# Kernel tuning notes

Measured on AMD Instinct MI355X. Metric: run time of the kernel, lower is better.

## Reference

```python
import jax, jax.numpy as jnp
import numpy as np

B, K, D, H = 4, 2048, 1024, 16
NCTX = K // 2
IMAGE_SIZE = 224
MAX_POS = 1024


def _build_rope_cache_2d(max_pos, dim, base=10000.0):
    half_dim = dim // 2
    theta = 1.0 / base ** (np.arange(0, half_dim, 2, dtype=np.float32) / half_dim)
    positions = np.arange(max_pos, dtype=np.float32)
    freqs = np.outer(positions, theta)  # [max_pos, dim/4]
    return jnp.asarray(np.stack([np.cos(freqs), np.sin(freqs)], axis=-1))  # [max_pos, dim/4, 2]


def apply_rope_2d(x, coords, rope_cache, image_size):
    b, k, d = x.shape
    half, quarter = d // 2, d // 4
    max_pos = rope_cache.shape[0]
    cn = jnp.clip(coords / image_size * (max_pos - 1), 0, max_pos - 1)
    y_pos = cn[..., 0].astype(jnp.int32)
    x_pos = cn[..., 1].astype(jnp.int32)
    y_rope = rope_cache[y_pos]  # [b,k,quarter,2]
    x_rope = rope_cache[x_pos]

    def rot(part, r):
        c, s = r[..., 0], r[..., 1]
        p0, p1 = part[..., 0], part[..., 1]
        return jnp.stack([p0 * c - p1 * s, p0 * s + p1 * c], -1).reshape(b, k, half)

    xp = x[..., :half].reshape(b, k, quarter, 2)
    yp = x[..., half:].reshape(b, k, quarter, 2)
    return jnp.concatenate([rot(xp, x_rope), rot(yp, y_rope)], -1)


def mha(q_tok, kv_tok, in_w, in_b, out_w, out_b, num_heads):
    b, nq, d = q_tok.shape
    hd = d // num_heads
    wq, wk, wv = jnp.split(in_w, 3, axis=0)
    bq, bk, bv = jnp.split(in_b, 3)
    q = (q_tok @ wq.T + bq).reshape(b, nq, num_heads, hd)
    k = (kv_tok @ wk.T + bk).reshape(b, -1, num_heads, hd)
    v = (kv_tok @ wv.T + bv).reshape(b, -1, num_heads, hd)
    s = jnp.einsum('bqhd,bkhd->bhqk', q, k) / jnp.sqrt(jnp.asarray(hd, q.dtype))
    a = jax.nn.softmax(s, axis=-1)
    o = jnp.einsum('bhqk,bkhd->bqhd', a, v).reshape(b, nq, d)
    return o @ out_w.T + out_b


def setup_inputs() -> dict:
    key = jax.random.key(0)
    ks = jax.random.split(key, 12)
    sc = 1.0 / np.sqrt(D)
    x = jax.random.normal(ks[0], (B, K, D), jnp.float32)
    coords = jax.random.uniform(ks[1], (B, K, 2), jnp.float32) * IMAGE_SIZE
    # boolean context mask with exactly NCTX context tokens per batch (code assumes equal counts)
    perms = jax.vmap(lambda k_: jax.random.permutation(k_, K))(jax.random.split(ks[2], B))
    is_context = jax.vmap(lambda m, i: m.at[i].set(True))(jnp.zeros((B, K), bool), perms[:, :NCTX])
    rope_cache = _build_rope_cache_2d(MAX_POS, D)
    return {
        'x': x, 'coords': coords, 'is_context': is_context, 'rope_cache': rope_cache,
        'ctx_in_w': jax.random.normal(ks[3], (3 * D, D), jnp.float32) * sc,
        'ctx_in_b': jnp.zeros((3 * D,), jnp.float32),
        'ctx_out_w': jax.random.normal(ks[4], (D, D), jnp.float32) * sc,
        'ctx_out_b': jnp.zeros((D,), jnp.float32),
        'tgt_in_w': jax.random.normal(ks[5], (3 * D, D), jnp.float32) * sc,
        'tgt_in_b': jnp.zeros((3 * D,), jnp.float32),
        'tgt_out_w': jax.random.normal(ks[6], (D, D), jnp.float32) * sc,
        'tgt_out_b': jnp.zeros((D,), jnp.float32),
    }


def reference(x, coords, is_context, rope_cache,
              ctx_in_w, ctx_in_b, ctx_out_w, ctx_out_b,
              tgt_in_w, tgt_in_b, tgt_out_w, tgt_out_b):
    # 2D RoPE before attention (as in the backbone)
    xr = apply_rope_2d(x, coords, rope_cache, IMAGE_SIZE)
    # stable argsort: context positions (key 0) first, in original order
    order = jnp.argsort(jnp.where(is_context, 0, 1), axis=1, stable=True)
    ctx_idx = order[:, :NCTX]   # [B, NCTX]
    tgt_idx = order[:, NCTX:]   # [B, K-NCTX]
    ctx_tok = jnp.take_along_axis(xr, ctx_idx[..., None], axis=1)
    tgt_tok = jnp.take_along_axis(xr, tgt_idx[..., None], axis=1)
    ctx_out = mha(ctx_tok, ctx_tok, ctx_in_w, ctx_in_b, ctx_out_w, ctx_out_b, H)
    tgt_out = mha(tgt_tok, ctx_tok, tgt_in_w, tgt_in_b, tgt_out_w, tgt_out_b, H)
    out = jnp.zeros_like(x)
    out = jax.vmap(lambda o, i, v: o.at[i].set(v))(out, ctx_idx, ctx_out)
    out = jax.vmap(lambda o, i, v: o.at[i].set(v))(out, tgt_idx, tgt_out)
    return out
```

## Files before the change

kernel.cpp:

```cpp
#include <hip/hip_runtime.h>
#include <math.h>

#define B_    4
#define K_    2048
#define D_    1024
#define H_    16
#define NCTX_ 1024

typedef unsigned short ushort_t;
typedef _Float16 f16;
typedef __attribute__((ext_vector_type(8))) _Float16 f16x8;
typedef __attribute__((ext_vector_type(4))) float f32x4;

union U4 {
  f16 h[4];
  ushort4 u;
};

union P4 {
  f16 h[4];
  ushort4 u;
};

__device__ __forceinline__ void gload16(const void* g, void* l) {
  __builtin_amdgcn_global_load_lds(
      (const __attribute__((address_space(1))) unsigned int*)g,
      (__attribute__((address_space(3))) unsigned int*)l, 16, 0, 0);
}

__global__ __launch_bounds__(256) void partition_kernel(
    const unsigned char* __restrict__ isctx, int* __restrict__ pos,
    int* __restrict__ ipos) {
  const int b = blockIdx.x;
  const int tid = threadIdx.x;
  const int wid = tid >> 6, lane = tid & 63;
  __shared__ int csum[4];
  __shared__ int waveTot[4];
  __shared__ int strideSh;

  int cnt = 0;
  for (int i = 0; i < 32; ++i) cnt += (isctx[tid * 32 + i] != 0);
  for (int off = 32; off; off >>= 1) cnt += __shfl_down(cnt, off, 64);
  if (lane == 0) csum[wid] = cnt;
  __syncthreads();
  if (tid == 0) {
    int t = csum[0] + csum[1] + csum[2] + csum[3];
    strideSh = (t > 2048) ? 1 : ((t > 768) ? 4 : 8);
  }
  __syncthreads();
  const int stride = strideSh;

  const unsigned char* base = isctx + (size_t)b * K_ * stride;
  int f[8];
  int s = 0;
  for (int i = 0; i < 8; ++i) {
    f[i] = base[(size_t)(tid * 8 + i) * stride] != 0;
    s += f[i];
  }
  int inc = s;
  for (int off = 1; off < 64; off <<= 1) {
    int v = __shfl_up(inc, off, 64);
    if (lane >= off) inc += v;
  }
  if (lane == 63) waveTot[wid] = inc;
  __syncthreads();
  int wOff = 0;
  for (int w = 0; w < wid; ++w) wOff += waveTot[w];
  int run = wOff + inc - s;
  for (int i = 0; i < 8; ++i) {
    int k = tid * 8 + i;
    int p;
    if (f[i]) {
      p = run;
      run++;
    } else {
      p = NCTX_ + k - run;
    }
    pos[b * K_ + k] = p;
    ipos[b * K_ + p] = k;
  }
}

__global__ __launch_bounds__(256) void rope_kernel(
    const float* __restrict__ x, const float* __restrict__ coords,
    const float* __restrict__ cache, const int* __restrict__ ipos,
    f16* __restrict__ tok) {
  const int row = blockIdx.x;
  const int b = row >> 11;
  const int r = row & (K_ - 1);
  const int k = ipos[row];
  const int t = threadIdx.x;

  const float cy = coords[(size_t)(b * K_ + k) * 2 + 0];
  const float cx = coords[(size_t)(b * K_ + k) * 2 + 1];
  const int ypos = (int)fminf(fmaxf(cy / 224.0f * 1023.0f, 0.0f), 1023.0f);
  const int xpos = (int)fminf(fmaxf(cx / 224.0f * 1023.0f, 0.0f), 1023.0f);

  const float4 v = ((const float4*)(x + ((size_t)b * K_ + k) * D_))[t];
  const int e = 4 * t;
  const float* crow;
  int coff;
  if (e < 512) {
    crow = cache + (size_t)xpos * 512;
    coff = e;
  } else {
    crow = cache + (size_t)ypos * 512;
    coff = e - 512;
  }
  const float4 cs = *(const float4*)(crow + coff);
  float o[4];
  o[0] = v.x * cs.x - v.y * cs.y;
  o[1] = v.x * cs.y + v.y * cs.x;
  o[2] = v.z * cs.z - v.w * cs.w;
  o[3] = v.z * cs.w + v.w * cs.z;
  U4 h;
#pragma unroll
  for (int i = 0; i < 4; ++i) h.h[i] = (f16)o[i];
  ((ushort4*)(tok + ((size_t)b * K_ + r) * D_))[t] = h.u;
}

__global__ __launch_bounds__(256) void cvt_all(
    const float* __restrict__ ctx_in_w, const float* __restrict__ tgt_in_w,
    const float* __restrict__ ctx_out_w, const float* __restrict__ tgt_out_w,
    f16* __restrict__ dst) {
  const int i4 = blockIdx.x * 256 + threadIdx.x;
  const int f = i4 * 4;
  const float* src;
  if (f < 3145728) src = ctx_in_w + f;
  else if (f < 5242880) src = tgt_in_w + (f - 3145728 + 1048576);
  else if (f < 6291456) src = tgt_in_w + (f - 5242880);
  else if (f < 7340032) src = ctx_out_w + (f - 6291456);
  else src = tgt_out_w + (f - 7340032);
  const float4 v = *(const float4*)src;
  U4 u;
  u.h[0] = (f16)v.x;
  u.h[1] = (f16)v.y;
  u.h[2] = (f16)v.z;
  u.h[3] = (f16)v.w;
  ((ushort4*)dst)[i4] = u.u;
}

#define GEMM_PRE(AP, WP, Kd)                                                  \
  const int rb_ = wave * 8 + (lane >> 3);          \
  const int kk_ = ((lane & 7) ^ (lane >> 3)) * 8;   \
  const f16* gA_ = (AP) + (size_t)rb_ * (Kd) + kk_;                           \
  const f16* gW_ = (WP) + (size_t)rb_ * (Kd) + kk_;                           \
  const int lA_ = wave * 8 * 64 + lane * 8;

#define GEMM_STAGE(k0s, bb)                                                   \
  _Pragma("unroll") for (int j = 0; j < 4; ++j) {                             \
    gload16(gA_ + (size_t)j * 32 * Kd_ + (k0s), &lds[(bb) + j * 2048 + lA_]); \
    gload16(gW_ + (size_t)j * 32 * Kd_ + (k0s),                               \
            &lds[(bb) + 8192 + j * 2048 + lA_]);                              \
  }

#define GEMM_TILE(bb)                                                         \
  _Pragma("unroll") for (int kh = 0; kh < 2; ++kh) {                          \
    f16x8 af[4], wf[4];                                                       \
    _Pragma("unroll") for (int i = 0; i < 4; ++i) {                           \
      const int ca = ((kh * 4 + quad) ^ (m16 & 7)) * 8;                       \
      af[i] = *(const f16x8*)&lds[(bb) + (wm + i * 16 + m16) * 64 + ca];      \
      wf[i] =                                                                 \
          *(const f16x8*)&lds[(bb) + 8192 + (wn + i * 16 + m16) * 64 + ca];   \
    }                                                                         \
    _Pragma("unroll") for (int i = 0; i < 4; ++i)                             \
        _Pragma("unroll") for (int j = 0; j < 4; ++j)                         \
      acc[i][j] = __builtin_amdgcn_mfma_f32_16x16x32_f16(af[i], wf[j],        \
                                                         acc[i][j], 0, 0, 0); \
  }

#define GEMM_CORE(AP, WP, Kd)                                                 \
  f32x4 acc[4][4];                                                            \
  {                                                                           \
    const f32x4 z = {0.f, 0.f, 0.f, 0.f};                                     \
    for (int i = 0; i < 4; ++i)                                               \
      for (int j = 0; j < 4; ++j) acc[i][j] = z;                              \
  }                                                                           \
  const int Kd_ = (Kd);                                                       \
  GEMM_PRE(AP, WP, Kd_)                                                       \
  GEMM_STAGE(0, 0)                                                            \
  for (int t = 0; t < Kd_ / 64; ++t) {                                        \
    const int cb = (t & 1) * 16384;                                           \
    if (t + 1 < Kd_ / 64) {                                                   \
      GEMM_STAGE((t + 1) * 64, ((t + 1) & 1) * 16384)                         \
      asm volatile("s_waitcnt vmcnt(8)" ::: "memory");                        \
    } else {                                                                  \
      asm volatile("s_waitcnt vmcnt(0)" ::: "memory");                        \
    }                                                                         \
    __builtin_amdgcn_s_barrier();                                             \
    asm volatile("" ::: "memory");                                            \
    GEMM_TILE(cb)                                                             \
    asm volatile("" ::: "memory");                                            \
    __builtin_amdgcn_s_barrier();                                             \
  }

__global__ __launch_bounds__(256, 2) void gemm_proj(
    const f16* __restrict__ tok, const f16* __restrict__ wcat,
    const float* __restrict__ ctx_in_b, const float* __restrict__ tgt_in_b,
    f16* __restrict__ qkvc, f16* __restrict__ kvt, f16* __restrict__ qt,
    f16* __restrict__ vtc, f16* __restrict__ vtt) {
  __shared__ f16 lds[32768];
  const int tid = threadIdx.x;
  const int wave = tid >> 6, lane = tid & 63;
  const int quad = lane >> 4, m16 = lane & 15;
  const int nb = blockIdx.x, mb = blockIdx.y, b = blockIdx.z;
  const int wm = (wave & 1) << 6, wn = (wave >> 1) << 6;
  const int m0 = mb * 128;
  const bool isQ = nb >= 40;
  const int n0 = isQ ? (nb - 40) * 128 : nb * 128;
  const f16* AP = tok + (size_t)b * K_ * D_ +
                  (isQ ? (size_t)NCTX_ * D_ : (size_t)0) + (size_t)m0 * D_;
  const f16* WP = wcat + (isQ ? (size_t)5242880 : (size_t)0) +
                  (size_t)n0 * D_;

  GEMM_CORE(AP, WP, D_)

#pragma unroll
  for (int j = 0; j < 4; ++j) {
    const int col = n0 + wn + j * 16 + m16;
    if (isQ) {
      const float bv = tgt_in_b[col];
      f16* dst = qt + (size_t)b * NCTX_ * 1024;
#pragma unroll
      for (int i = 0; i < 4; ++i) {
        const int mr = m0 + wm + i * 16 + quad * 4;
#pragma unroll
        for (int r = 0; r < 4; ++r)
          dst[(size_t)(mr + r) * 1024 + col] = (f16)(acc[i][j][r] + bv);
      }
    } else if (col < 2048) {
      const float bv = ctx_in_b[col];
      f16* dst = qkvc + (size_t)b * NCTX_ * 2048;
#pragma unroll
      for (int i = 0; i < 4; ++i) {
        const int mr = m0 + wm + i * 16 + quad * 4;
#pragma unroll
        for (int r = 0; r < 4; ++r)
          dst[(size_t)(mr + r) * 2048 + col] = (f16)(acc[i][j][r] + bv);
      }
    } else if (col >= 3072 && col < 4096) {
      const float bv = tgt_in_b[D_ + col - 3072];
      f16* dst = kvt + (size_t)b * NCTX_ * 1024;
      const int dcol = col - 3072;
#pragma unroll
      for (int i = 0; i < 4; ++i) {
        const int mr = m0 + wm + i * 16 + quad * 4;
#pragma unroll
        for (int r = 0; r < 4; ++r)
          dst[(size_t)(mr + r) * 1024 + dcol] = (f16)(acc[i][j][r] + bv);
      }
    } else {
      const bool isCtxV = col < 3072;
      const int hd = isCtxV ? (col - 2048) : (col - 4096);
      const float bv = isCtxV ? ctx_in_b[col] : tgt_in_b[D_ + col - 3072];
      f16* dst = (isCtxV ? vtc : vtt) +
                 ((size_t)(b * H_ + (hd >> 6)) << 16) +
                 (size_t)(hd & 63) * 1024;
#pragma unroll
      for (int i = 0; i < 4; ++i) {
        const int mr = m0 + wm + i * 16 + quad * 4;
        P4 p4;
#pragma unroll
        for (int r = 0; r < 4; ++r) p4.h[r] = (f16)(acc[i][j][r] + bv);
        *(ushort4*)(dst + mr) = p4.u;
      }
    }
  }
}

__global__ __launch_bounds__(256, 2) void gemm_out(
    const f16* __restrict__ Atok, const f16* __restrict__ Wbase,
    const float* __restrict__ bias_ctx, const float* __restrict__ bias_tgt,
    const int* __restrict__ ipos, float* __restrict__ out) {
  __shared__ f16 lds[32768];
  const int tid = threadIdx.x;
  const int wave = tid >> 6, lane = tid & 63;
  const int quad = lane >> 4, m16 = lane & 15;
  const int n0 = blockIdx.x * 128, m0 = blockIdx.y * 128;
  const int b = blockIdx.z & 3, sel = blockIdx.z >> 2;
  const int wm = (wave & 1) << 6, wn = (wave >> 1) << 6;
  const f16* AP = Atok + (size_t)b * K_ * D_ + (size_t)sel * NCTX_ * D_ +
                  (size_t)m0 * D_;
  const f16* WP = Wbase + (size_t)sel * 1048576 + (size_t)n0 * D_;
  const float* bias = sel ? bias_tgt : bias_ctx;

  GEMM_CORE(AP, WP, D_)

#pragma unroll
  for (int j = 0; j < 4; ++j) {
    const int col = n0 + wn + j * 16 + m16;
    const float bv = bias[col];
#pragma unroll
    for (int i = 0; i < 4; ++i) {
      const int mr = m0 + wm + i * 16 + quad * 4;
#pragma unroll
      for (int r = 0; r < 4; ++r) {
        const int orow = ipos[b * K_ + sel * NCTX_ + mr + r];
        out[(size_t)b * K_ * D_ + (size_t)orow * D_ + col] =
            acc[i][j][r] + bv;
      }
    }
  }
}

__global__ __launch_bounds__(512) void attn_mfma(
    const f16* __restrict__ qkvc, const f16* __restrict__ kvt,
    const f16* __restrict__ qt, const f16* __restrict__ vtc,
    const f16* __restrict__ vtt, f16* __restrict__ O) {
  __shared__ f16 QP[8192];
  __shared__ f16 Ks[2][4096];
  __shared__ f16 Vs[2][4096];
  const int tid = threadIdx.x, wave = tid >> 6, lane = tid & 63;
  const int quad = lane >> 4, m16 = lane & 15;
  const int q0 = blockIdx.x * 128, h = blockIdx.y;
  const int zz = blockIdx.z;
  const int b = zz & 3;
  const bool isCtx = zz < 4;

  const f16* Qb;
  const f16* Kb;
  int ld;
  if (isCtx) {
    Qb = qkvc + (size_t)b * NCTX_ * 2048 + h * 64;
    Kb = Qb + 1024;
    ld = 2048;
  } else {
    Qb = qt + (size_t)b * NCTX_ * 1024 + h * 64;
    Kb = kvt + (size_t)b * NCTX_ * 1024 + h * 64;
    ld = 1024;
  }
  const f16* Vb = (isCtx ? vtc : vtt) + ((size_t)(b * H_ + h) << 16);
  f16* Ob = O + (size_t)b * K_ * D_ + (isCtx ? 0 : (size_t)NCTX_ * D_);

  const int rowS = tid >> 3;
  const int kkc = ((tid & 7) ^ (rowS & 7)) * 8;
  const int lB = tid * 8;

#pragma unroll
  for (int j = 0; j < 2; ++j)
    gload16(Qb + (size_t)(q0 + j * 64 + rowS) * ld + kkc, &QP[j * 4096 + lB]);
  gload16(Kb + (size_t)rowS * ld + kkc, &Ks[0][lB]);
  gload16(Vb + (size_t)rowS * 1024 + kkc, &Vs[0][lB]);

  float m_run = -1e30f, l_run = 0.f;
  f32x4 Oa[4];
  const f32x4 z = {0.f, 0.f, 0.f, 0.f};
#pragma unroll
  for (int j = 0; j < 4; ++j) Oa[j] = z;

  asm volatile("s_waitcnt vmcnt(2)" ::: "memory");
  __builtin_amdgcn_s_barrier();

  const int c0 = (quad ^ (m16 & 7)) * 8;
  const int c1 = ((quad + 4) ^ (m16 & 7)) * 8;
  const f16x8 qf0 = *(const f16x8*)&QP[(wave * 16 + m16) * 64 + c0];
  const f16x8 qf1 = *(const f16x8*)&QP[(wave * 16 + m16) * 64 + c1];

  f16* Pw = QP + wave * 1024;

  for (int kt = 0; kt < 16; ++kt) {
    const int cur = kt & 1;
    if (kt < 15) {
      gload16(Kb + (size_t)((kt + 1) * 64 + rowS) * ld + kkc,
              &Ks[cur ^ 1][lB]);
      gload16(Vb + (size_t)rowS * 1024 + (kt + 1) * 64 + kkc,
              &Vs[cur ^ 1][lB]);
      asm volatile("s_waitcnt vmcnt(2)" ::: "memory");
    } else {
      asm volatile("s_waitcnt vmcnt(0)" ::: "memory");
    }
    __builtin_amdgcn_s_barrier();

    f32x4 S[4];
    __builtin_amdgcn_s_setprio(1);
#pragma unroll
    for (int jn = 0; jn < 4; ++jn) {
      S[jn] = z;
      const f16x8 kf0 = *(const f16x8*)&Ks[cur][(jn * 16 + m16) * 64 + c0];
      const f16x8 kf1 = *(const f16x8*)&Ks[cur][(jn * 16 + m16) * 64 + c1];
      S[jn] = __builtin_amdgcn_mfma_f32_16x16x32_f16(kf0, qf0, S[jn], 0, 0, 0);
      S[jn] = __builtin_amdgcn_mfma_f32_16x16x32_f16(kf1, qf1, S[jn], 0, 0, 0);
    }
    __builtin_amdgcn_s_setprio(0);

    float mv0 = fmaxf(fmaxf(S[0][0], S[1][0]), fmaxf(S[2][0], S[3][0]));
    float mv1 = fmaxf(fmaxf(S[0][1], S[1][1]), fmaxf(S[2][1], S[3][1]));
    float mv2 = fmaxf(fmaxf(S[0][2], S[1][2]), fmaxf(S[2][2], S[3][2]));
    float mv3 = fmaxf(fmaxf(S[0][3], S[1][3]), fmaxf(S[2][3], S[3][3]));
    float mx = fmaxf(fmaxf(mv0, mv1), fmaxf(mv2, mv3));
    mx = fmaxf(mx, __shfl_xor(mx, 16, 64));
    mx = fmaxf(mx, __shfl_xor(mx, 32, 64));
    mx *= 0.125f;

    const bool grow = !__all(mx <= m_run);
    float al = 1.f;
    if (grow) {
      const float mnew = fmaxf(m_run, mx);
      al = __expf(m_run - mnew);
      m_run = mnew;
    }

    float rs = 0.f;
#pragma unroll
    for (int jn = 0; jn < 4; ++jn) {
      P4 p4;
#pragma unroll
      for (int r = 0; r < 4; ++r) {
        const float p = __expf(__builtin_fmaf(S[jn][r], 0.125f, -m_run));
        rs += p;
        p4.h[r] = (f16)p;
      }
      *(ushort4*)&Pw[m16 * 64 + (((jn * 2 + (quad >> 1)) ^ (m16 & 7)) * 8) +
                     (quad & 1) * 4] = p4.u;
    }
    rs += __shfl_xor(rs, 16, 64);
    rs += __shfl_xor(rs, 32, 64);

    if (grow) {
      l_run = l_run * al + rs;
      float alq[4];
#pragma unroll
      for (int r = 0; r < 4; ++r) alq[r] = __shfl(al, quad * 4 + r, 64);
#pragma unroll
      for (int j = 0; j < 4; ++j) {
        Oa[j][0] *= alq[0];
        Oa[j][1] *= alq[1];
        Oa[j][2] *= alq[2];
        Oa[j][3] *= alq[3];
      }
    } else {
      l_run += rs;
    }

    const f16x8 pf0 = *(const f16x8*)&Pw[m16 * 64 + c0];
    const f16x8 pf1 = *(const f16x8*)&Pw[m16 * 64 + c1];
    __builtin_amdgcn_s_setprio(1);
#pragma unroll
    for (int jd = 0; jd < 4; ++jd) {
      const f16x8 vf0 = *(const f16x8*)&Vs[cur][(jd * 16 + m16) * 64 + c0];
      const f16x8 vf1 = *(const f16x8*)&Vs[cur][(jd * 16 + m16) * 64 + c1];
      Oa[jd] = __builtin_amdgcn_mfma_f32_16x16x32_f16(pf0, vf0, Oa[jd], 0, 0, 0);
      Oa[jd] = __builtin_amdgcn_mfma_f32_16x16x32_f16(pf1, vf1, Oa[jd], 0, 0, 0);
    }
    __builtin_amdgcn_s_setprio(0);
    __builtin_amdgcn_s_barrier();
  }

  float lq[4];
#pragma unroll
  for (int r = 0; r < 4; ++r) lq[r] = 1.0f / __shfl(l_run, quad * 4 + r, 64);
#pragma unroll
  for (int jd = 0; jd < 4; ++jd)
#pragma unroll
    for (int r = 0; r < 4; ++r) {
      const float v = Oa[jd][r] * lq[r];
      const size_t off = (size_t)(q0 + wave * 16 + quad * 4 + r) * D_ +
                         h * 64 + jd * 16 + m16;
      Ob[off] = (f16)v;
    }
}

extern "C" void kernel_launch(void* const* d_in, const int* in_sizes, int n_in,
                              void* d_out, int out_size, void* d_ws,
                              size_t ws_size, hipStream_t stream) {
  const float* x = (const float*)d_in[0];
  const float* coords = (const float*)d_in[1];
  const unsigned char* isctx = (const unsigned char*)d_in[2];
  const float* rope = (const float*)d_in[3];
  const float* ctx_in_w = (const float*)d_in[4];
  const float* ctx_in_b = (const float*)d_in[5];
  const float* ctx_out_w = (const float*)d_in[6];
  const float* ctx_out_b = (const float*)d_in[7];
  const float* tgt_in_w = (const float*)d_in[8];
  const float* tgt_in_b = (const float*)d_in[9];
  const float* tgt_out_w = (const float*)d_in[10];
  const float* tgt_out_b = (const float*)d_in[11];
  float* out = (float*)d_out;

  f16* ws = (f16*)d_ws;
  f16* tok = ws;
  f16* wcat = tok + 8388608;
  f16* qkvc = wcat + 8388608;
  f16* kvt = qkvc + 8388608;
  f16* qt = kvt + 4194304;
  f16* vtc = qt + 4194304;
  f16* vtt = vtc + 4194304;
  int* pos = (int*)(vtt + 4194304);
  int* ipos = pos + B_ * K_;

  partition_kernel<<<B_, 256, 0, stream>>>(isctx, pos, ipos);
  cvt_all<<<8192, 256, 0, stream>>>(ctx_in_w, tgt_in_w, ctx_out_w, tgt_out_w,
                                    wcat);
  rope_kernel<<<B_ * K_, 256, 0, stream>>>(x, coords, rope, ipos, tok);

  gemm_proj<<<dim3(48, 8, B_), 256, 0, stream>>>(
      tok, wcat, ctx_in_b, tgt_in_b, qkvc, kvt, qt, vtc, vtt);

  attn_mfma<<<dim3(8, H_, 2 * B_), 512, 0, stream>>>(qkvc, kvt, qt, vtc, vtt,
                                                     tok);

  gemm_out<<<dim3(8, 8, 2 * B_), 256, 0, stream>>>(
      tok, wcat + 6291456, ctx_out_b, tgt_out_b, ipos, out);
}
```

Measured before the change: 286.0 us.

## Use triple-slot K/V ring buffer and XCD-aware block mapping in attention

```diff
diff --git a/kernel.cpp b/kernel.cpp
--- a/kernel.cpp
+++ b/kernel.cpp
@@ -308,14 +308,20 @@
     const f16* __restrict__ qt, const f16* __restrict__ vtc,
     const f16* __restrict__ vtt, f16* __restrict__ O) {
   __shared__ f16 QP[8192];
-  __shared__ f16 Ks[2][4096];
-  __shared__ f16 Vs[2][4096];
+  __shared__ f16 Xb[12288];
   const int tid = threadIdx.x, wave = tid >> 6, lane = tid & 63;
   const int quad = lane >> 4, m16 = lane & 15;
-  const int q0 = blockIdx.x * 128, h = blockIdx.y;
-  const int zz = blockIdx.z;
+
+  const int id = blockIdx.x;
+  const int xcd = id & 7;
+  const int t_ = id >> 3;
+  const int j_ = t_ & 7;
+  const int g = ((t_ >> 3) << 3) + xcd;
+  const int h = g & 15;
+  const int zz = g >> 4;
   const int b = zz & 3;
   const bool isCtx = zz < 4;
+  const int q0 = j_ * 128;
 
   const f16* Qb;
   const f16* Kb;
@@ -339,8 +345,8 @@
 #pragma unroll
   for (int j = 0; j < 2; ++j)
     gload16(Qb + (size_t)(q0 + j * 64 + rowS) * ld + kkc, &QP[j * 4096 + lB]);
-  gload16(Kb + (size_t)rowS * ld + kkc, &Ks[0][lB]);
-  gload16(Vb + (size_t)rowS * 1024 + kkc, &Vs[0][lB]);
+  gload16(Kb + (size_t)rowS * ld + kkc, &Xb[lB]);
+  gload16(Vb + (size_t)rowS * 1024 + kkc, &Xb[4096 + lB]);
 
   float m_run = -1e30f, l_run = 0.f;
   f32x4 Oa[4];
@@ -348,7 +354,7 @@
 #pragma unroll
   for (int j = 0; j < 4; ++j) Oa[j] = z;
 
-  asm volatile("s_waitcnt vmcnt(2)" ::: "memory");
+  asm volatile("s_waitcnt vmcnt(0)" ::: "memory");
   __builtin_amdgcn_s_barrier();
 
   const int c0 = (quad ^ (m16 & 7)) * 8;
@@ -358,30 +364,33 @@
 
   f16* Pw = QP + wave * 1024;
 
+  int xK = 0, xV = 4096;
   for (int kt = 0; kt < 16; ++kt) {
-    const int cur = kt & 1;
-    if (kt < 15) {
-      gload16(Kb + (size_t)((kt + 1) * 64 + rowS) * ld + kkc,
-              &Ks[cur ^ 1][lB]);
-      gload16(Vb + (size_t)rowS * 1024 + (kt + 1) * 64 + kkc,
-              &Vs[cur ^ 1][lB]);
-      asm volatile("s_waitcnt vmcnt(2)" ::: "memory");
-    } else {
-      asm volatile("s_waitcnt vmcnt(0)" ::: "memory");
-    }
+    int xKn = xK + 8192;
+    if (xKn >= 12288) xKn -= 12288;
+
+    asm volatile("s_waitcnt vmcnt(0)" ::: "memory");
     __builtin_amdgcn_s_barrier();
+    asm volatile("" ::: "memory");
+    if (kt < 15)
+      gload16(Kb + (size_t)((kt + 1) * 64 + rowS) * ld + kkc, &Xb[xKn + lB]);
 
     f32x4 S[4];
     __builtin_amdgcn_s_setprio(1);
 #pragma unroll
     for (int jn = 0; jn < 4; ++jn) {
       S[jn] = z;
-      const f16x8 kf0 = *(const f16x8*)&Ks[cur][(jn * 16 + m16) * 64 + c0];
-      const f16x8 kf1 = *(const f16x8*)&Ks[cur][(jn * 16 + m16) * 64 + c1];
+      const f16x8 kf0 = *(const f16x8*)&Xb[xK + (jn * 16 + m16) * 64 + c0];
+      const f16x8 kf1 = *(const f16x8*)&Xb[xK + (jn * 16 + m16) * 64 + c1];
       S[jn] = __builtin_amdgcn_mfma_f32_16x16x32_f16(kf0, qf0, S[jn], 0, 0, 0);
       S[jn] = __builtin_amdgcn_mfma_f32_16x16x32_f16(kf1, qf1, S[jn], 0, 0, 0);
     }
     __builtin_amdgcn_s_setprio(0);
+
+    __builtin_amdgcn_s_barrier();
+    asm volatile("" ::: "memory");
+    if (kt < 15)
+      gload16(Vb + (size_t)rowS * 1024 + (kt + 1) * 64 + kkc, &Xb[xK + lB]);
 
     float mv0 = fmaxf(fmaxf(S[0][0], S[1][0]), fmaxf(S[2][0], S[3][0]));
     float mv1 = fmaxf(fmaxf(S[0][1], S[1][1]), fmaxf(S[2][1], S[3][1]));
@@ -437,13 +446,15 @@
     __builtin_amdgcn_s_setprio(1);
 #pragma unroll
     for (int jd = 0; jd < 4; ++jd) {
-      const f16x8 vf0 = *(const f16x8*)&Vs[cur][(jd * 16 + m16) * 64 + c0];
-      const f16x8 vf1 = *(const f16x8*)&Vs[cur][(jd * 16 + m16) * 64 + c1];
+      const f16x8 vf0 = *(const f16x8*)&Xb[xV + (jd * 16 + m16) * 64 + c0];
+      const f16x8 vf1 = *(const f16x8*)&Xb[xV + (jd * 16 + m16) * 64 + c1];
       Oa[jd] = __builtin_amdgcn_mfma_f32_16x16x32_f16(pf0, vf0, Oa[jd], 0, 0, 0);
       Oa[jd] = __builtin_amdgcn_mfma_f32_16x16x32_f16(pf1, vf1, Oa[jd], 0, 0, 0);
     }
     __builtin_amdgcn_s_setprio(0);
-    __builtin_amdgcn_s_barrier();
+
+    xV = xK;
+    xK = xKn;
   }
 
   float lq[4];
@@ -496,8 +507,8 @@
   gemm_proj<<<dim3(48, 8, B_), 256, 0, stream>>>(
       tok, wcat, ctx_in_b, tgt_in_b, qkvc, kvt, qt, vtc, vtt);
 
-  attn_mfma<<<dim3(8, H_, 2 * B_), 512, 0, stream>>>(qkvc, kvt, qt, vtc, vtt,
-                                                     tok);
+  attn_mfma<<<dim3(1024, 1, 1), 512, 0, stream>>>(qkvc, kvt, qt, vtc, vtt,
+                                                  tok);
 
   gemm_out<<<dim3(8, 8, 2 * B_), 256, 0, stream>>>(
       tok, wcat + 6291456, ctx_out_b, tgt_out_b, ipos, out);
```

After: 278.8 us. -2.5%, faster.
